# Kernel optimization log

Hardware: AMD Instinct MI355X
Metric: run time of the kernel (lower is better)

## Reference

```python
import jax, jax.numpy as jnp
import numpy as np
import math

EMSIZE = 256
NHEAD = 8
HEAD = EMSIZE // NHEAD
SEQ = 2048
BATCH = 2


def setup_inputs() -> dict:
    key = jax.random.key(0)
    ks = jax.random.split(key, 8)
    s = 1.0 / math.sqrt(EMSIZE)
    return {
        "em": jax.random.normal(ks[0], (SEQ, BATCH, EMSIZE), jnp.float32),
        "mask": jnp.zeros((BATCH, 1, SEQ, SEQ), jnp.float32),
        "Wq": jax.random.normal(ks[1], (EMSIZE, EMSIZE), jnp.float32) * s,
        "bq": jnp.zeros((EMSIZE,), jnp.float32),
        "Wk": jax.random.normal(ks[2], (EMSIZE, EMSIZE), jnp.float32) * s,
        "bk": jnp.zeros((EMSIZE,), jnp.float32),
        "Wv": jax.random.normal(ks[3], (EMSIZE, EMSIZE), jnp.float32) * s,
        "bv": jnp.zeros((EMSIZE,), jnp.float32),
    }


def reference(em, mask, Wq, bq, Wk, bk, Wv, bv):
    # em: [S, B, E] -> [B, S, E]
    x = jnp.swapaxes(em, 0, 1)
    B, S, E = x.shape
    H, D = NHEAD, HEAD
    # QKV projections (nn.Linear: x @ W.T + b), split heads -> [B, S, H, D]
    q = (x @ Wq.T + bq).reshape(B, S, H, D)
    k = (x @ Wk.T + bk).reshape(B, S, H, D)
    v = (x @ Wv.T + bv).reshape(B, S, H, D)
    # scores: [B, H, S, S]
    scores = jnp.einsum("bqhd,bkhd->bhqk", q, k) / math.sqrt(D) + mask
    attn = jax.nn.softmax(scores, axis=-1)  # dropout in eval mode = identity
    # context: [B, S, H, D] -> [B, S, E] -> [S, B, E]
    ctx = jnp.einsum("bhqk,bkhd->bqhd", attn, v).reshape(B, S, E)
    return jnp.swapaxes(ctx, 0, 1)
```

## Files before the change

kernel.cpp:

```cpp
#include <hip/hip_runtime.h>
#include <hip/hip_bf16.h>

typedef float f32x4 __attribute__((ext_vector_type(4)));
typedef float f32x16 __attribute__((ext_vector_type(16)));
typedef __bf16 bf16x8 __attribute__((ext_vector_type(8)));
typedef int v2i __attribute__((ext_vector_type(2)));
typedef unsigned short ushort_t;

#define SEQ 2048
#define BATCH 2
#define EMS 256
#define NHEAD 8
#define HEAD 32
#define BH (BATCH*NHEAD)
#define LOG2E 1.4426950408889634f
#define QSCALE 0.2550348211f
#define THRS 11.5415603f

static __device__ __forceinline__ ushort_t f2bfbits(float f) {
    unsigned int u = __float_as_uint(f);
    u += 0x7fffu + ((u >> 16) & 1u);
    return (ushort_t)(u >> 16);
}

static __device__ __forceinline__ unsigned cvtpk(float lo, float hi) {
    unsigned r;
    asm("v_cvt_pk_bf16_f32 %0, %1, %2" : "=v"(r) : "v"(lo), "v"(hi));
    return r;
}

static __device__ __forceinline__ float exp2a(float x) {
    float r;
    asm("v_exp_f32 %0, %1" : "=v"(r) : "v"(x));
    return r;
}

static __device__ __forceinline__ bf16x8 cvt8(const float* p) {
    float4 a = *reinterpret_cast<const float4*>(p);
    float4 b = *reinterpret_cast<const float4*>(p + 4);
    union { bf16x8 v; uint4 u; } x;
    x.u.x = cvtpk(a.x, a.y);
    x.u.y = cvtpk(a.z, a.w);
    x.u.z = cvtpk(b.x, b.y);
    x.u.w = cvtpk(b.z, b.w);
    return x.v;
}

__global__ __launch_bounds__(256) void fused_pre(
    const float* __restrict__ em, const float* __restrict__ mask,
    const float* __restrict__ Wq, const float* __restrict__ bq,
    const float* __restrict__ Wk, const float* __restrict__ bk,
    const float* __restrict__ Wv, const float* __restrict__ bv,
    ushort_t* __restrict__ Qb, ushort_t* __restrict__ Kb,
    ushort_t* __restrict__ Vt2, unsigned long long* __restrict__ flagsG)
{
    if (blockIdx.x < 1024) {
        int fb = blockIdx.x;
        int kq = fb & 3, qt = (fb >> 2) & 127, b = fb >> 9;
        int t = threadIdx.x;
        int r = t >> 4, i = t & 15;
        const float* base = mask + ((size_t)b * SEQ + qt * 16 + r) * SEQ + kq * 512 + i * 4;
        unsigned nzb = 0;
        #pragma unroll
        for (int j = 0; j < 8; j++) {
            float4 v = *(const float4*)(base + j * 64);
            unsigned u = (__float_as_uint(v.x) | __float_as_uint(v.y) |
                          __float_as_uint(v.z) | __float_as_uint(v.w)) << 1;
            if (u) nzb |= 1u << (2 * j + (i >> 3));
        }
        __shared__ unsigned fl;
        if (t == 0) fl = 0;
        __syncthreads();
        if (nzb) atomicOr(&fl, nzb);
        __syncthreads();
        if (t == 0) ((ushort_t*)flagsG)[(b * 128 + qt) * 4 + kq] = (ushort_t)fl;
        return;
    }

    int wid = (blockIdx.x - 1024) * 4 + (threadIdx.x >> 6);
    int l   = threadIdx.x & 63;
    int l15 = l & 15, lq = l >> 4;
    int rb = wid / 24, cg = wid % 24;
    int r0 = rb * 32, c0 = cg * 32;
    int sel = c0 >> 8;
    const float* W    = sel == 0 ? Wq : (sel == 1 ? Wk : Wv);
    const float* bias = sel == 0 ? bq : (sel == 1 ? bk : bv);
    int cb = c0 & 255;

    f32x4 acc[2][2];
    #pragma unroll
    for (int m = 0; m < 2; m++)
        #pragma unroll
        for (int n = 0; n < 2; n++) acc[m][n] = (f32x4){0.f, 0.f, 0.f, 0.f};

    #pragma unroll
    for (int kk = 0; kk < 8; kk++) {
        int k0 = kk * 32;
        bf16x8 af[2], bfm[2];
        #pragma unroll
        for (int m = 0; m < 2; m++)
            af[m] = cvt8(em + (size_t)(r0 + m * 16 + l15) * EMS + k0 + lq * 8);
        #pragma unroll
        for (int n = 0; n < 2; n++)
            bfm[n] = cvt8(W + (size_t)(cb + n * 16 + l15) * EMS + k0 + lq * 8);
        #pragma unroll
        for (int m = 0; m < 2; m++)
            #pragma unroll
            for (int n = 0; n < 2; n++)
                acc[m][n] = __builtin_amdgcn_mfma_f32_16x16x32_bf16(af[m], bfm[n], acc[m][n], 0, 0, 0);
    }

    float scale = (sel == 0) ? QSCALE : 1.0f;
    #pragma unroll
    for (int m = 0; m < 2; m++) {
        #pragma unroll
        for (int n = 0; n < 2; n++) {
            int c = cb + n * 16 + l15;
            float bv_ = bias[c];
            int h = c >> 5, d = c & 31;
            #pragma unroll
            for (int r = 0; r < 4; r++) {
                int row = r0 + m * 16 + lq * 4 + r;
                int s = row >> 1, b = row & 1;
                int bh = b * NHEAD + h;
                ushort_t v = f2bfbits((acc[m][n][r] + bv_) * scale);
                if (sel == 0)      Qb[((size_t)bh * SEQ + s) * HEAD + d] = v;
                else if (sel == 1) Kb[((size_t)bh * SEQ + s) * HEAD + d] = v;
                else               Vt2[(((size_t)bh * 64 + (s >> 5)) * 32 + d) * 32 + (s & 31)] = v;
            }
        }
    }
}

__global__ __launch_bounds__(256, 4) void attn(
    const ushort_t* __restrict__ Qb, const ushort_t* __restrict__ Kb,
    const ushort_t* __restrict__ Vt2, const float* __restrict__ mask,
    const unsigned long long* __restrict__ flagsG, float* __restrict__ out)
{
    int g  = blockIdx.x;
    int qt = g >> 4;
    int b  = (g >> 3) & 1;
    int h  = g & 7;
    int bh = b * NHEAD + h;
    int w  = threadIdx.x >> 6;
    int l  = threadIdx.x & 63;
    int l31 = l & 31, hi = l >> 5;
    int qs0 = qt * 32;

    __shared__ float oacc[4][32][36];
    __shared__ float om[4][32], ol[4][32];

    const ushort_t* qrow = Qb + ((size_t)bh * SEQ + qs0 + l31) * HEAD + hi * 8;
    bf16x8 qf0 = *(const bf16x8*)(qrow);
    bf16x8 qf1 = *(const bf16x8*)(qrow + 16);

    unsigned long long fbits = flagsG[b * 128 + qt * 2] | flagsG[b * 128 + qt * 2 + 1];

    f32x16 acc = {};
    float mrun = -1e30f, lsum = 0.f;

    int k0 = w * (SEQ / 4);
    const ushort_t* kbase = Kb  + ((size_t)bh * SEQ + k0 + l31) * HEAD + hi * 8;
    const ushort_t* vbase = Vt2 + ((size_t)bh * 64 + (k0 >> 5)) * 1024 + l31 * 32 + hi * 8;

    bf16x8 kc0 = *(const bf16x8*)(kbase);
    bf16x8 kc1 = *(const bf16x8*)(kbase + 16);
    bf16x8 vc0 = *(const bf16x8*)(vbase);
    bf16x8 vc1 = *(const bf16x8*)(vbase + 16);

    const int NT = (SEQ / 4) / 32;
    for (int kt = 0; kt < NT; kt++) {
        int ktn = (kt + 1 < NT) ? kt + 1 : 0;
        f32x16 st = {};
        st = __builtin_amdgcn_mfma_f32_32x32x16_bf16(kc0, qf0, st, 0, 0, 0);
        st = __builtin_amdgcn_mfma_f32_32x32x16_bf16(kc1, qf1, st, 0, 0, 0);

        bf16x8 kn0 = *(const bf16x8*)(kbase + ktn * 1024);
        bf16x8 kn1 = *(const bf16x8*)(kbase + ktn * 1024 + 16);
        bf16x8 vn0 = *(const bf16x8*)(vbase + ktn * 1024);
        bf16x8 vn1 = *(const bf16x8*)(vbase + ktn * 1024 + 16);

        if ((fbits >> (w * 16 + kt)) & 1ull) {
            const float* mr = mask + (size_t)b * SEQ * SEQ
                            + (size_t)(qs0 + l31) * SEQ + k0 + kt * 32 + hi * 4;
            union { float4 f4[4]; float f[16]; } mu;
            mu.f4[0] = *(const float4*)(mr);
            mu.f4[1] = *(const float4*)(mr + 8);
            mu.f4[2] = *(const float4*)(mr + 16);
            mu.f4[3] = *(const float4*)(mr + 24);
            #pragma unroll
            for (int j = 0; j < 16; j++) st[j] += mu.f[j] * LOG2E;
        }

        float x0 = fmaxf(st[0], st[1]),  x1 = fmaxf(st[2], st[3]);
        float x2 = fmaxf(st[4], st[5]),  x3 = fmaxf(st[6], st[7]);
        float x4 = fmaxf(st[8], st[9]),  x5 = fmaxf(st[10], st[11]);
        float x6 = fmaxf(st[12], st[13]), x7 = fmaxf(st[14], st[15]);
        float lmax = fmaxf(fmaxf(fmaxf(x0, x1), fmaxf(x2, x3)),
                           fmaxf(fmaxf(x4, x5), fmaxf(x6, x7)));

        if (__any(lmax > mrun + THRS)) {
            v2i sw = __builtin_amdgcn_permlane32_swap(
                __float_as_int(lmax), __float_as_int(lmax), false, false);
            float pm = fmaxf(fmaxf(lmax, __int_as_float(sw.x)), __int_as_float(sw.y));
            float nm = fmaxf(mrun, pm);
            float sc = exp2a(mrun - nm);
            lsum *= sc;
            #pragma unroll
            for (int j = 0; j < 16; j++) acc[j] *= sc;
            mrun = nm;
        }

        float ev[16];
        #pragma unroll
        for (int j = 0; j < 16; j++) ev[j] = exp2a(st[j] - mrun);
        lsum += (((ev[0]+ev[1])+(ev[2]+ev[3])) + ((ev[4]+ev[5])+(ev[6]+ev[7])))
              + (((ev[8]+ev[9])+(ev[10]+ev[11])) + ((ev[12]+ev[13])+(ev[14]+ev[15])));

        unsigned pk[8];
        #pragma unroll
        for (int j = 0; j < 8; j++) pk[j] = cvtpk(ev[2 * j], ev[2 * j + 1]);
        v2i p0 = __builtin_amdgcn_permlane32_swap((int)pk[0], (int)pk[2], false, false);
        v2i p1 = __builtin_amdgcn_permlane32_swap((int)pk[1], (int)pk[3], false, false);
        v2i p2 = __builtin_amdgcn_permlane32_swap((int)pk[4], (int)pk[6], false, false);
        v2i p3 = __builtin_amdgcn_permlane32_swap((int)pk[5], (int)pk[7], false, false);
        union { int i[4]; bf16x8 v; } pf0, pf1;
        pf0.i[0] = p0.x; pf0.i[1] = p1.x; pf0.i[2] = p0.y; pf0.i[3] = p1.y;
        pf1.i[0] = p2.x; pf1.i[1] = p3.x; pf1.i[2] = p2.y; pf1.i[3] = p3.y;

        acc = __builtin_amdgcn_mfma_f32_32x32x16_bf16(vc0, pf0.v, acc, 0, 0, 0);
        acc = __builtin_amdgcn_mfma_f32_32x32x16_bf16(vc1, pf1.v, acc, 0, 0, 0);

        kc0 = kn0; kc1 = kn1; vc0 = vn0; vc1 = vn1;
    }

    v2i sl = __builtin_amdgcn_permlane32_swap(
        __float_as_int(lsum), __float_as_int(lsum), false, false);
    float lt = __int_as_float(sl.x) + __int_as_float(sl.y);
    if (hi == 0) { om[w][l31] = mrun; ol[w][l31] = lt; }

    #pragma unroll
    for (int gg = 0; gg < 4; gg++) {
        f32x4 vv = { acc[4*gg], acc[4*gg+1], acc[4*gg+2], acc[4*gg+3] };
        *(f32x4*)&oacc[w][l31][8 * gg + 4 * hi] = vv;
    }
    __syncthreads();

    int t = threadIdx.x;
    int q = t >> 3, d4 = (t & 7) * 4;
    float m0 = om[0][q], m1 = om[1][q], m2 = om[2][q], m3 = om[3][q];
    float mg = fmaxf(fmaxf(m0, m1), fmaxf(m2, m3));
    float w0_ = exp2a(m0 - mg), w1_ = exp2a(m1 - mg);
    float w2_ = exp2a(m2 - mg), w3_ = exp2a(m3 - mg);
    float lg = w0_ * ol[0][q] + w1_ * ol[1][q] + w2_ * ol[2][q] + w3_ * ol[3][q];
    float inv = 1.0f / lg;
    float4 o;
    o.x = (w0_*oacc[0][q][d4]   + w1_*oacc[1][q][d4]   + w2_*oacc[2][q][d4]   + w3_*oacc[3][q][d4])   * inv;
    o.y = (w0_*oacc[0][q][d4+1] + w1_*oacc[1][q][d4+1] + w2_*oacc[2][q][d4+1] + w3_*oacc[3][q][d4+1]) * inv;
    o.z = (w0_*oacc[0][q][d4+2] + w1_*oacc[1][q][d4+2] + w2_*oacc[2][q][d4+2] + w3_*oacc[3][q][d4+2]) * inv;
    o.w = (w0_*oacc[0][q][d4+3] + w1_*oacc[1][q][d4+3] + w2_*oacc[2][q][d4+3] + w3_*oacc[3][q][d4+3]) * inv;
    *(float4*)(out + ((size_t)(qs0 + q) * BATCH + b) * EMS + h * HEAD + d4) = o;
}

extern "C" void kernel_launch(void* const* d_in, const int* in_sizes, int n_in,
                              void* d_out, int out_size, void* d_ws, size_t ws_size,
                              hipStream_t stream) {
    const float* em  = (const float*)d_in[0];
    const float* mask = (const float*)d_in[1];
    const float* Wq  = (const float*)d_in[2];
    const float* bq  = (const float*)d_in[3];
    const float* Wk  = (const float*)d_in[4];
    const float* bk  = (const float*)d_in[5];
    const float* Wv  = (const float*)d_in[6];
    const float* bv  = (const float*)d_in[7];
    float* out = (float*)d_out;

    ushort_t* Qb  = (ushort_t*)d_ws;
    ushort_t* Kb  = Qb + (size_t)BH * SEQ * HEAD;
    ushort_t* Vt2 = Kb + (size_t)BH * SEQ * HEAD;
    unsigned long long* flagsG = (unsigned long long*)(Vt2 + (size_t)BH * SEQ * HEAD);

    fused_pre<<<dim3(1792), dim3(256), 0, stream>>>(em, mask, Wq, bq, Wk, bk, Wv, bv,
                                                    Qb, Kb, Vt2, flagsG);
    attn<<<dim3(1024), dim3(256), 0, stream>>>(Qb, Kb, Vt2, mask, flagsG, out);
}
```

Measured before the change: 54.18 us.

## Move V transpose to a separate kernel, widen projection tiles, coarsen mask scan

The QKV projection now writes V in the same row-major head layout as Q and K. A new small kernel then transposes V through shared memory into the blocked layout the attention kernel expects, replacing the scattered strided stores of the old epilogue. Each projection warp now computes a 32x64 tile instead of 32x32, reusing the em fragments across more columns. Mask-scan blocks each cover 16 rows by 1024 columns with row-wise coalesced loads, while keeping the same bitmask layout. The cost is an extra kernel launch and an extra round trip of V through global memory.

```diff
diff --git a/kernel.cpp b/kernel.cpp
--- a/kernel.cpp
+++ b/kernel.cpp
@@ -52,61 +52,61 @@
     const float* __restrict__ Wk, const float* __restrict__ bk,
     const float* __restrict__ Wv, const float* __restrict__ bv,
     ushort_t* __restrict__ Qb, ushort_t* __restrict__ Kb,
-    ushort_t* __restrict__ Vt2, unsigned long long* __restrict__ flagsG)
+    ushort_t* __restrict__ Vb, unsigned* __restrict__ flagsG)
 {
-    if (blockIdx.x < 1024) {
-        int fb = blockIdx.x;
-        int kq = fb & 3, qt = (fb >> 2) & 127, b = fb >> 9;
+    if (blockIdx.x >= 384) {
+        int sb = blockIdx.x - 384;
+        int kh = sb & 1, qt = (sb >> 1) & 127, b = sb >> 8;
         int t = threadIdx.x;
-        int r = t >> 4, i = t & 15;
-        const float* base = mask + ((size_t)b * SEQ + qt * 16 + r) * SEQ + kq * 512 + i * 4;
-        unsigned nzb = 0;
-        #pragma unroll
-        for (int j = 0; j < 8; j++) {
-            float4 v = *(const float4*)(base + j * 64);
+        const float* base = mask + ((size_t)b * SEQ + qt * 16) * SEQ + kh * 1024 + t * 4;
+        unsigned nz = 0;
+        #pragma unroll 4
+        for (int it = 0; it < 16; it++) {
+            float4 v = *(const float4*)(base + (size_t)it * SEQ);
             unsigned u = (__float_as_uint(v.x) | __float_as_uint(v.y) |
                           __float_as_uint(v.z) | __float_as_uint(v.w)) << 1;
-            if (u) nzb |= 1u << (2 * j + (i >> 3));
+            if (u) nz = 1;
         }
         __shared__ unsigned fl;
         if (t == 0) fl = 0;
         __syncthreads();
-        if (nzb) atomicOr(&fl, nzb);
+        if (nz) atomicOr(&fl, 1u << (t >> 3));
         __syncthreads();
-        if (t == 0) ((ushort_t*)flagsG)[(b * 128 + qt) * 4 + kq] = (ushort_t)fl;
+        if (t == 0) flagsG[(b * 128 + qt) * 2 + kh] = fl;
         return;
     }
 
-    int wid = (blockIdx.x - 1024) * 4 + (threadIdx.x >> 6);
+    int wid = blockIdx.x * 4 + (threadIdx.x >> 6);
     int l   = threadIdx.x & 63;
     int l15 = l & 15, lq = l >> 4;
-    int rb = wid / 24, cg = wid % 24;
-    int r0 = rb * 32, c0 = cg * 32;
+    int rb = wid / 12, cg = wid % 12;
+    int r0 = rb * 32, c0 = cg * 64;
     int sel = c0 >> 8;
     const float* W    = sel == 0 ? Wq : (sel == 1 ? Wk : Wv);
     const float* bias = sel == 0 ? bq : (sel == 1 ? bk : bv);
+    ushort_t*    dst  = sel == 0 ? Qb : (sel == 1 ? Kb : Vb);
     int cb = c0 & 255;
 
-    f32x4 acc[2][2];
+    f32x4 acc[2][4];
     #pragma unroll
     for (int m = 0; m < 2; m++)
         #pragma unroll
-        for (int n = 0; n < 2; n++) acc[m][n] = (f32x4){0.f, 0.f, 0.f, 0.f};
+        for (int n = 0; n < 4; n++) acc[m][n] = (f32x4){0.f, 0.f, 0.f, 0.f};
 
     #pragma unroll
     for (int kk = 0; kk < 8; kk++) {
         int k0 = kk * 32;
-        bf16x8 af[2], bfm[2];
+        bf16x8 af[2], bfm[4];
         #pragma unroll
         for (int m = 0; m < 2; m++)
             af[m] = cvt8(em + (size_t)(r0 + m * 16 + l15) * EMS + k0 + lq * 8);
         #pragma unroll
-        for (int n = 0; n < 2; n++)
+        for (int n = 0; n < 4; n++)
             bfm[n] = cvt8(W + (size_t)(cb + n * 16 + l15) * EMS + k0 + lq * 8);
         #pragma unroll
         for (int m = 0; m < 2; m++)
             #pragma unroll
-            for (int n = 0; n < 2; n++)
+            for (int n = 0; n < 4; n++)
                 acc[m][n] = __builtin_amdgcn_mfma_f32_16x16x32_bf16(af[m], bfm[n], acc[m][n], 0, 0, 0);
     }
 
@@ -114,7 +114,7 @@
     #pragma unroll
     for (int m = 0; m < 2; m++) {
         #pragma unroll
-        for (int n = 0; n < 2; n++) {
+        for (int n = 0; n < 4; n++) {
             int c = cb + n * 16 + l15;
             float bv_ = bias[c];
             int h = c >> 5, d = c & 31;
@@ -122,13 +122,34 @@
             for (int r = 0; r < 4; r++) {
                 int row = r0 + m * 16 + lq * 4 + r;
                 int s = row >> 1, b = row & 1;
-                int bh = b * NHEAD + h;
                 ushort_t v = f2bfbits((acc[m][n][r] + bv_) * scale);
-                if (sel == 0)      Qb[((size_t)bh * SEQ + s) * HEAD + d] = v;
-                else if (sel == 1) Kb[((size_t)bh * SEQ + s) * HEAD + d] = v;
-                else               Vt2[(((size_t)bh * 64 + (s >> 5)) * 32 + d) * 32 + (s & 31)] = v;
+                dst[((size_t)(b * NHEAD + h) * SEQ + s) * HEAD + d] = v;
             }
         }
+    }
+}
+
+__global__ __launch_bounds__(256) void vtrans(const ushort_t* __restrict__ Vb,
+                                              ushort_t* __restrict__ Vt2)
+{
+    __shared__ ushort_t t[HEAD][65];
+    int g = blockIdx.x;
+    int bh = g & 15, st = g >> 4;
+    int s0 = st * 64;
+    int tid = threadIdx.x;
+    #pragma unroll
+    for (int i = 0; i < 8; i++) {
+        int idx = i * 256 + tid;
+        int sl = idx >> 5, d = idx & 31;
+        t[d][sl] = Vb[((size_t)bh * SEQ + s0 + sl) * HEAD + d];
+    }
+    __syncthreads();
+    #pragma unroll
+    for (int i = 0; i < 8; i++) {
+        int idx = i * 256 + tid;
+        int kb_l = idx >> 10, rem = idx & 1023;
+        int d = rem >> 5, si = rem & 31;
+        Vt2[(((size_t)bh * 64 + (s0 >> 5) + kb_l) * 32 + d) * 32 + si] = t[d][kb_l * 32 + si];
     }
 }
 
@@ -277,10 +298,13 @@
 
     ushort_t* Qb  = (ushort_t*)d_ws;
     ushort_t* Kb  = Qb + (size_t)BH * SEQ * HEAD;
-    ushort_t* Vt2 = Kb + (size_t)BH * SEQ * HEAD;
-    unsigned long long* flagsG = (unsigned long long*)(Vt2 + (size_t)BH * SEQ * HEAD);
-
-    fused_pre<<<dim3(1792), dim3(256), 0, stream>>>(em, mask, Wq, bq, Wk, bk, Wv, bv,
-                                                    Qb, Kb, Vt2, flagsG);
-    attn<<<dim3(1024), dim3(256), 0, stream>>>(Qb, Kb, Vt2, mask, flagsG, out);
-}
+    ushort_t* Vb  = Kb + (size_t)BH * SEQ * HEAD;
+    ushort_t* Vt2 = Vb + (size_t)BH * SEQ * HEAD;
+    unsigned* flagsG = (unsigned*)(Vt2 + (size_t)BH * SEQ * HEAD);
+
+    fused_pre<<<dim3(896), dim3(256), 0, stream>>>(em, mask, Wq, bq, Wk, bk, Wv, bv,
+                                                   Qb, Kb, Vb, flagsG);
+    vtrans<<<dim3(512), dim3(256), 0, stream>>>(Vb, Vt2);
+    attn<<<dim3(1024), dim3(256), 0, stream>>>(Qb, Kb, Vt2, mask,
+                                               (const unsigned long long*)flagsG, out);
+}
```

Measured after the change: 51.71 us. -4.6%, faster.
